# Optimization experiments

Measured on AMD Instinct MI355X. Metric: run time of the kernel, lower is better.

## Reference

```python
import jax, jax.numpy as jnp
import numpy as np

B, T, D, K = 32, 2048, 1024, 31


def setup_inputs() -> dict:
    key = jax.random.key(0)
    ks = jax.random.split(key, 8)
    query = jax.random.normal(ks[0], (B, D), dtype=jnp.float32)
    memory = jax.random.normal(ks[1], (B, T, D), dtype=jnp.float32)
    prev_attn = jax.nn.softmax(jax.random.normal(ks[2], (B, T)), axis=-1).astype(jnp.float32)
    cum_attn = jax.random.uniform(ks[3], (B, T), dtype=jnp.float32)
    mask = jax.random.bernoulli(ks[4], 0.2, (B, T))
    mask = mask.at[:, 0].set(False)  # keep at least one valid position per row
    scale = 0.02
    Wq = jax.random.normal(ks[5], (D, D), dtype=jnp.float32) * scale    # torch Linear weight [out,in]
    Wm = jax.random.normal(ks[6], (D, D), dtype=jnp.float32) * scale
    k2 = jax.random.split(ks[7], 2)
    Wloc = jax.random.normal(k2[0], (D, 2, K), dtype=jnp.float32) * scale  # Conv1d weight [out_ch,in_ch,k]
    v = jax.random.normal(k2[1], (D,), dtype=jnp.float32) * scale          # Linear(d_model,1) weight squeezed
    return {"query": query, "memory": memory, "prev_attn": prev_attn,
            "cum_attn": cum_attn, "mask": mask,
            "Wq": Wq, "Wm": Wm, "Wloc": Wloc, "v": v}


def reference(query, memory, prev_attn, cum_attn, mask, Wq, Wm, Wloc, v):
    pad = Wloc.shape[-1] // 2
    # location features: [B,2,T] conv -> [B,D,T] -> [B,T,D]
    loc_in = jnp.stack([prev_attn, cum_attn], axis=1)
    loc = jax.lax.conv_general_dilated(
        loc_in, Wloc, window_strides=(1,), padding=[(pad, pad)],
        dimension_numbers=("NCW", "OIW", "NCW"))
    loc = jnp.transpose(loc, (0, 2, 1))                 # [B,T,D]
    q = (query @ Wq.T)[:, None, :]                      # [B,1,D]
    m = jnp.einsum("btd,ed->bte", memory, Wm)           # [B,T,D]
    e = jnp.einsum("btd,d->bt", jnp.tanh(q + m + loc), v)  # [B,T]
    e = jnp.where(mask, -jnp.inf, e)
    a = jax.nn.softmax(e, axis=1)                       # [B,T]
    ctx = jnp.einsum("bt,btd->bd", a, memory)           # [B,D]
    return ctx, a
```

## Files before the change

kernel.cpp:

```cpp
#include <hip/hip_runtime.h>
#include <math.h>

#define BATCH 32
#define T 2048
#define D 1024
#define KW 31
#define CPAD 15
#define KEXT 62
#define KTOT 1088
#define BM 256
#define BN 256
#define KSTEP 64
#define NK (KTOT / KSTEP)

typedef __bf16 bf16_8 __attribute__((ext_vector_type(8)));
typedef __bf16 bf16_4 __attribute__((ext_vector_type(4)));
typedef float  f32x4  __attribute__((ext_vector_type(4)));

__device__ __forceinline__ float tanh_fast(float x) {
    return 1.f - 2.f * __builtin_amdgcn_rcpf(__expf(2.f * x) + 1.f);
}

__device__ __forceinline__ void glds16(const void* gsrc, void* ldst) {
    __builtin_amdgcn_global_load_lds(
        (const __attribute__((address_space(1))) unsigned int*)gsrc,
        (__attribute__((address_space(3))) unsigned int*)ldst, 16, 0, 0);
}

#define VM4 asm volatile("s_waitcnt vmcnt(4)" ::: "memory")
#define VM0 asm volatile("s_waitcnt vmcnt(0)" ::: "memory")
#define BAR __builtin_amdgcn_s_barrier()
#define PRIO1 __builtin_amdgcn_s_setprio(1)
#define PRIO0 __builtin_amdgcn_s_setprio(0)

__global__ __launch_bounds__(256) void k_prep_b(const float* __restrict__ Wm,
                                                const float* __restrict__ Wloc,
                                                __bf16* __restrict__ Bext) {
    const int idx = blockIdx.x * 256 + threadIdx.x;
    const int d = idx / (KTOT / 4);
    const int kk = (idx % (KTOT / 4)) * 4;
    bf16_4 o;
    #pragma unroll
    for (int u = 0; u < 4; ++u) {
        const int k = kk + u;
        float val = 0.f;
        if (k < D) val = Wm[(size_t)d * D + k];
        else {
            const int j = k - D;
            if (j < KEXT) {
                const int c = (j >= KW) ? 1 : 0;
                const int kp = j - c * KW;
                val = Wloc[((size_t)d * 2 + c) * KW + kp];
            }
        }
        o[u] = (__bf16)val;
    }
    *(bf16_4*)(Bext + (size_t)d * KTOT + kk) = o;
}

__global__ __launch_bounds__(256) void k_prep_amem(const float* __restrict__ memory,
                                                   __bf16* __restrict__ Amem) {
    const int nvec = BATCH * T * (D / 16);
    for (int idx = blockIdx.x * 256 + threadIdx.x; idx < nvec; idx += gridDim.x * 256) {
        const int row = idx >> 6;
        const int c = (idx & 63) * 16;
        const float* src = memory + (size_t)row * D + c;
        const f32x4 a0 = *(const f32x4*)(src);
        const f32x4 a1 = *(const f32x4*)(src + 4);
        const f32x4 a2 = *(const f32x4*)(src + 8);
        const f32x4 a3 = *(const f32x4*)(src + 12);
        bf16_8 o0, o1;
        #pragma unroll
        for (int u = 0; u < 4; ++u) {
            o0[u] = (__bf16)a0[u]; o0[u + 4] = (__bf16)a1[u];
            o1[u] = (__bf16)a2[u]; o1[u + 4] = (__bf16)a3[u];
        }
        __bf16* dst = Amem + (size_t)row * KTOT + c;
        *(bf16_8*)(dst) = o0;
        *(bf16_8*)(dst + 8) = o1;
    }
}

__global__ __launch_bounds__(256) void k_prep_aloc(const float* __restrict__ prev,
                                                   const float* __restrict__ cum,
                                                   __bf16* __restrict__ Amem) {
    const int idx = blockIdx.x * 256 + threadIdx.x;
    const int row = idx >> 4;
    const int j0 = (idx & 15) * 4;
    const int b = row >> 11;
    const int t = row & (T - 1);
    bf16_4 o;
    #pragma unroll
    for (int u = 0; u < 4; ++u) {
        const int j = j0 + u;
        float val = 0.f;
        if (j < KEXT) {
            const int c = (j >= KW) ? 1 : 0;
            const int kp = j - c * KW;
            const int ts = t + kp - CPAD;
            if (ts >= 0 && ts < T)
                val = (c ? cum : prev)[(size_t)b * T + ts];
        }
        o[u] = (__bf16)val;
    }
    *(bf16_4*)(Amem + (size_t)row * KTOT + D + j0) = o;
}

__global__ __launch_bounds__(256) void k_q(const float* __restrict__ query,
                                           const float* __restrict__ Wq,
                                           float* __restrict__ qout) {
    int b = blockIdx.y;
    int w = threadIdx.x >> 6;
    int lane = threadIdx.x & 63;
    int d = blockIdx.x * 4 + w;
    const float* qrow = query + (size_t)b * D;
    const float* wrow = Wq + (size_t)d * D;
    float s = 0.f;
    #pragma unroll
    for (int i = 0; i < D / 64; ++i) s += qrow[lane + i * 64] * wrow[lane + i * 64];
    #pragma unroll
    for (int off = 32; off > 0; off >>= 1) s += __shfl_down(s, off, 64);
    if (lane == 0) qout[(size_t)b * D + d] = s;
}

__global__ __launch_bounds__(512, 2) void k_gemm_e(
    const __bf16* __restrict__ Amem, const __bf16* __restrict__ Bext,
    const float* __restrict__ qv, const float* __restrict__ vvec,
    float* __restrict__ e_part) {
    __shared__ bf16_8 As[2][2048];
    __shared__ bf16_8 Bs[2][2048];

    const int t0 = blockIdx.x * BM;
    const int d0 = blockIdx.y * BN;
    const int b  = blockIdx.z;
    const int tid  = threadIdx.x;
    const int lane = tid & 63;
    const int w    = tid >> 6;
    const int wm   = w >> 2;
    const int wn   = w & 3;
    const int ml   = lane & 15;
    const int qk   = lane >> 4;

    f32x4 acc[8][4] = {};

    const __bf16* gA[2][2];
    const __bf16* gB[2][2];
    int sA[2][2], sB[2][2];
    #pragma unroll
    for (int h = 0; h < 2; ++h) {
        #pragma unroll
        for (int j = 0; j < 2; ++j) {
            const int idx = j * 8 + w;
            const int p = idx >> 1, kfa = idx & 1;
            const int mf = h * 4 + (p & 3) + (idx & 8);
            const int nf = h * 2 + (p & 1) + (p >> 1) * 4;
            gA[h][j] = Amem + ((size_t)b * T + t0 + mf * 16 + ml) * KTOT + kfa * 32 + qk * 8;
            sA[h][j] = (mf * 2 + kfa) * 64;
            gB[h][j] = Bext + (size_t)(d0 + nf * 16 + ml) * KTOT + kfa * 32 + qk * 8;
            sB[h][j] = (nf * 2 + kfa) * 64;
        }
    }

    bf16_8 areg[4][2];
    bf16_8 breg0[2][2], breg1[2][2];

    auto STG_A = [&](int h, int kcol, bf16_8* dst) {
        glds16(gA[h][0] + kcol, dst + sA[h][0]);
        glds16(gA[h][1] + kcol, dst + sA[h][1]);
    };
    auto STG_B = [&](int h, int kcol, bf16_8* dst) {
        glds16(gB[h][0] + kcol, dst + sB[h][0]);
        glds16(gB[h][1] + kcol, dst + sB[h][1]);
    };
    auto LDA = [&](const bf16_8* buf, int ih) {
        #pragma unroll
        for (int i = 0; i < 4; ++i)
            #pragma unroll
            for (int kf = 0; kf < 2; ++kf)
                areg[i][kf] = buf[((wm * 8 + ih * 4 + i) * 2 + kf) * 64 + lane];
    };
    auto LDB = [&](bf16_8 (&dst)[2][2], const bf16_8* buf, int jh) {
        #pragma unroll
        for (int j = 0; j < 2; ++j)
            #pragma unroll
            for (int kf = 0; kf < 2; ++kf)
                dst[j][kf] = buf[((wn * 4 + jh * 2 + j) * 2 + kf) * 64 + lane];
    };
    auto QMM = [&](bf16_8 (&bb)[2][2], int ih, int jh) {
        #pragma unroll
        for (int i = 0; i < 4; ++i)
            #pragma unroll
            for (int kf = 0; kf < 2; ++kf)
                #pragma unroll
                for (int j = 0; j < 2; ++j)
                    acc[ih * 4 + i][jh * 2 + j] = __builtin_amdgcn_mfma_f32_16x16x32_bf16(
                        areg[i][kf], bb[j][kf], acc[ih * 4 + i][jh * 2 + j], 0, 0, 0);
    };

    STG_A(0, 0, As[0]);
    STG_B(0, 0, Bs[0]);
    STG_B(1, 0, Bs[0]);
    STG_A(1, 0, As[0]);
    VM4;
    BAR;

    #pragma unroll 1
    for (int k = 0; k < NK; ++k) {
        const bf16_8* Ac = As[k & 1];
        const bf16_8* Bc = Bs[k & 1];
        bf16_8* An = As[(k + 1) & 1];
        bf16_8* Bn = Bs[(k + 1) & 1];
        const int c1 = ((k + 1 < NK) ? (k + 1) : 0) * KSTEP;
        LDA(Ac, 0);
        LDB(breg0, Bc, 0);
        STG_A(0, c1, An);
        BAR;
        PRIO1; QMM(breg0, 0, 0); PRIO0;
        VM4;
        BAR;
        LDB(breg1, Bc, 1);
        STG_B(0, c1, Bn);
        BAR;
        PRIO1; QMM(breg1, 0, 1); PRIO0;
        VM4;
        BAR;
        LDA(Ac, 1);
        STG_B(1, c1, Bn);
        BAR;
        PRIO1; QMM(breg0, 1, 0); PRIO0;
        BAR;
        STG_A(1, c1, An);
        BAR;
        PRIO1; QMM(breg1, 1, 1); PRIO0;
        VM4;
        BAR;
    }
    VM0;

    float qreg[4], vreg[4];
    #pragma unroll
    for (int jb = 0; jb < 4; ++jb) {
        const int d = d0 + wn * 64 + jb * 16 + ml;
        qreg[jb] = qv[(size_t)b * D + d];
        vreg[jb] = vvec[d];
    }
    const int dch = blockIdx.y * 4 + wn;
    #pragma unroll
    for (int ia = 0; ia < 8; ++ia) {
        #pragma unroll
        for (int r = 0; r < 4; ++r) {
            float s = 0.f;
            #pragma unroll
            for (int jb = 0; jb < 4; ++jb)
                s += tanh_fast(acc[ia][jb][r] + qreg[jb]) * vreg[jb];
            #pragma unroll
            for (int off = 8; off > 0; off >>= 1)
                s += __shfl_down(s, off, 16);
            if (ml == 0) {
                const int t = t0 + wm * 128 + ia * 16 + qk * 4 + r;
                e_part[((size_t)b * T + t) * 16 + dch] = s;
            }
        }
    }
}

__global__ __launch_bounds__(256) void k_softmax(const float* __restrict__ e_part,
                                                 const int* __restrict__ mask,
                                                 float* __restrict__ aout) {
    const int b = blockIdx.x;
    const int tid = threadIdx.x;
    __shared__ float red[256];
    float ev[8];
    float lmax = -INFINITY;
    #pragma unroll
    for (int i = 0; i < 8; ++i) {
        const int t = tid + i * 256;
        const float* p = e_part + ((size_t)b * T + t) * 16;
        float s = 0.f;
        #pragma unroll
        for (int c = 0; c < 16; ++c) s += p[c];
        if (mask[(size_t)b * T + t] != 0) s = -INFINITY;
        ev[i] = s;
        lmax = fmaxf(lmax, s);
    }
    red[tid] = lmax; __syncthreads();
    for (int off = 128; off > 0; off >>= 1) {
        if (tid < off) red[tid] = fmaxf(red[tid], red[tid + off]);
        __syncthreads();
    }
    const float mx = red[0]; __syncthreads();
    float lsum = 0.f;
    #pragma unroll
    for (int i = 0; i < 8; ++i) {
        const float x = expf(ev[i] - mx);
        ev[i] = x;
        lsum += x;
    }
    red[tid] = lsum; __syncthreads();
    for (int off = 128; off > 0; off >>= 1) {
        if (tid < off) red[tid] += red[tid + off];
        __syncthreads();
    }
    const float inv = 1.f / red[0];
    #pragma unroll
    for (int i = 0; i < 8; ++i)
        aout[(size_t)b * T + tid + i * 256] = ev[i] * inv;
}

__global__ __launch_bounds__(256) void k_ctx_part(const float* __restrict__ memory,
                                                  const float* __restrict__ a,
                                                  float* __restrict__ ctx_part) {
    const int b = blockIdx.x;
    const int tc = blockIdx.y;
    const int d4 = threadIdx.x * 4;
    f32x4 acc = {0.f, 0.f, 0.f, 0.f};
    const float* mb = memory + ((size_t)b * T + (size_t)tc * 64) * D;
    const float* ab = a + (size_t)b * T + (size_t)tc * 64;
    #pragma unroll 4
    for (int t = 0; t < 64; ++t) {
        const float wgt = ab[t];
        const f32x4 m4 = *(const f32x4*)(mb + (size_t)t * D + d4);
        acc += wgt * m4;
    }
    *(f32x4*)(ctx_part + ((size_t)(b * 32 + tc)) * D + d4) = acc;
}

__global__ __launch_bounds__(256) void k_ctx_red(const float* __restrict__ ctx_part,
                                                 float* __restrict__ ctx) {
    const int idx = blockIdx.x * 256 + threadIdx.x;
    const int b = idx >> 10, d = idx & 1023;
    float s = 0.f;
    #pragma unroll
    for (int tc = 0; tc < 32; ++tc) s += ctx_part[((size_t)(b * 32 + tc)) * D + d];
    ctx[idx] = s;
}

extern "C" void kernel_launch(void* const* d_in, const int* in_sizes, int n_in,
                              void* d_out, int out_size, void* d_ws, size_t ws_size,
                              hipStream_t stream) {
    const float* query  = (const float*)d_in[0];
    const float* memory = (const float*)d_in[1];
    const float* prev   = (const float*)d_in[2];
    const float* cum    = (const float*)d_in[3];
    const int*   mask   = (const int*)d_in[4];
    const float* Wq     = (const float*)d_in[5];
    const float* Wm     = (const float*)d_in[6];
    const float* Wloc   = (const float*)d_in[7];
    const float* v      = (const float*)d_in[8];

    float* out = (float*)d_out;
    float* ctx = out;
    float* a   = out + BATCH * D;

    char* ws = (char*)d_ws;
    float*  qv       = (float*)(ws + 0);
    float*  e_part   = (float*)(ws + 131072);
    float*  ctx_part = (float*)(ws + 4325376);
    __bf16* Bext     = (__bf16*)(ws + 8519680);
    __bf16* Amem     = (__bf16*)(ws + 10747904);

    k_prep_b<<<KTOT * D / (256 * 4), 256, 0, stream>>>(Wm, Wloc, Bext);
    k_prep_amem<<<4096, 256, 0, stream>>>(memory, Amem);
    k_prep_aloc<<<BATCH * T * 16 / 256, 256, 0, stream>>>(prev, cum, Amem);
    k_q<<<dim3(D / 4, BATCH), 256, 0, stream>>>(query, Wq, qv);
    k_gemm_e<<<dim3(T / BM, D / BN, BATCH), 512, 0, stream>>>(Amem, Bext, qv, v, e_part);
    k_softmax<<<BATCH, 256, 0, stream>>>(e_part, mask, a);
    k_ctx_part<<<dim3(BATCH, 32), 256, 0, stream>>>(memory, a, ctx_part);
    k_ctx_red<<<(BATCH * D) / 256, 256, 0, stream>>>(ctx_part, ctx);
}
```

Measured before the change: 686.1 us.

## Merge prep kernels, reduce e partials in LDS, read bf16 memory for ctx

Combines the four preprocessing kernels into one launch that dispatches on block index, removing three launches and their tail gaps. In the GEMM epilogue the four per-warp column partials are summed through shared memory, so only 4 partials per row are written instead of 16, and the softmax reads them as one vector. The context kernel now reads the bf16 copy of memory instead of fp32, halving its traffic. The cost is lower context precision and an extra barrier in the GEMM epilogue.

```diff
diff --git a/kernel.cpp b/kernel.cpp
--- a/kernel.cpp
+++ b/kernel.cpp
@@ -33,94 +33,93 @@
 #define PRIO1 __builtin_amdgcn_s_setprio(1)
 #define PRIO0 __builtin_amdgcn_s_setprio(0)
 
-__global__ __launch_bounds__(256) void k_prep_b(const float* __restrict__ Wm,
-                                                const float* __restrict__ Wloc,
-                                                __bf16* __restrict__ Bext) {
-    const int idx = blockIdx.x * 256 + threadIdx.x;
-    const int d = idx / (KTOT / 4);
-    const int kk = (idx % (KTOT / 4)) * 4;
-    bf16_4 o;
-    #pragma unroll
-    for (int u = 0; u < 4; ++u) {
-        const int k = kk + u;
-        float val = 0.f;
-        if (k < D) val = Wm[(size_t)d * D + k];
-        else {
-            const int j = k - D;
-            if (j < KEXT) {
-                const int c = (j >= KW) ? 1 : 0;
-                const int kp = j - c * KW;
-                val = Wloc[((size_t)d * 2 + c) * KW + kp];
+#define PREP_BLOCKS 17472
+__global__ __launch_bounds__(256) void k_prep_all(
+    const float* __restrict__ Wm, const float* __restrict__ Wloc,
+    __bf16* __restrict__ Bext,
+    const float* __restrict__ memory, __bf16* __restrict__ Amem,
+    const float* __restrict__ prev, const float* __restrict__ cum,
+    const float* __restrict__ query, const float* __restrict__ Wq,
+    float* __restrict__ qout) {
+    const int gb = blockIdx.x;
+    if (gb < 4096) {
+        const int nvec = BATCH * T * (D / 16);
+        for (int idx = gb * 256 + threadIdx.x; idx < nvec; idx += 4096 * 256) {
+            const int row = idx >> 6;
+            const int c = (idx & 63) * 16;
+            const float* src = memory + (size_t)row * D + c;
+            const f32x4 a0 = *(const f32x4*)(src);
+            const f32x4 a1 = *(const f32x4*)(src + 4);
+            const f32x4 a2 = *(const f32x4*)(src + 8);
+            const f32x4 a3 = *(const f32x4*)(src + 12);
+            bf16_8 o0, o1;
+            #pragma unroll
+            for (int u = 0; u < 4; ++u) {
+                o0[u] = (__bf16)a0[u]; o0[u + 4] = (__bf16)a1[u];
+                o1[u] = (__bf16)a2[u]; o1[u + 4] = (__bf16)a3[u];
             }
-        }
-        o[u] = (__bf16)val;
-    }
-    *(bf16_4*)(Bext + (size_t)d * KTOT + kk) = o;
-}
-
-__global__ __launch_bounds__(256) void k_prep_amem(const float* __restrict__ memory,
-                                                   __bf16* __restrict__ Amem) {
-    const int nvec = BATCH * T * (D / 16);
-    for (int idx = blockIdx.x * 256 + threadIdx.x; idx < nvec; idx += gridDim.x * 256) {
-        const int row = idx >> 6;
-        const int c = (idx & 63) * 16;
-        const float* src = memory + (size_t)row * D + c;
-        const f32x4 a0 = *(const f32x4*)(src);
-        const f32x4 a1 = *(const f32x4*)(src + 4);
-        const f32x4 a2 = *(const f32x4*)(src + 8);
-        const f32x4 a3 = *(const f32x4*)(src + 12);
-        bf16_8 o0, o1;
+            __bf16* dst = Amem + (size_t)row * KTOT + c;
+            *(bf16_8*)(dst) = o0;
+            *(bf16_8*)(dst + 8) = o1;
+        }
+    } else if (gb < 12288) {
+        const int j = gb - 4096;
+        const int xb = j & 255;
+        const int b = j >> 8;
+        const int w = threadIdx.x >> 6;
+        const int lane = threadIdx.x & 63;
+        const int d = xb * 4 + w;
+        const float* qrow = query + (size_t)b * D;
+        const float* wrow = Wq + (size_t)d * D;
+        float s = 0.f;
+        #pragma unroll
+        for (int i = 0; i < D / 64; ++i) s += qrow[lane + i * 64] * wrow[lane + i * 64];
+        #pragma unroll
+        for (int off = 32; off > 0; off >>= 1) s += __shfl_down(s, off, 64);
+        if (lane == 0) qout[(size_t)b * D + d] = s;
+    } else if (gb < 16384) {
+        const int idx = (gb - 12288) * 256 + threadIdx.x;
+        const int row = idx >> 4;
+        const int j0 = (idx & 15) * 4;
+        const int b = row >> 11;
+        const int t = row & (T - 1);
+        bf16_4 o;
         #pragma unroll
         for (int u = 0; u < 4; ++u) {
-            o0[u] = (__bf16)a0[u]; o0[u + 4] = (__bf16)a1[u];
-            o1[u] = (__bf16)a2[u]; o1[u + 4] = (__bf16)a3[u];
-        }
-        __bf16* dst = Amem + (size_t)row * KTOT + c;
-        *(bf16_8*)(dst) = o0;
-        *(bf16_8*)(dst + 8) = o1;
-    }
-}
-
-__global__ __launch_bounds__(256) void k_prep_aloc(const float* __restrict__ prev,
-                                                   const float* __restrict__ cum,
-                                                   __bf16* __restrict__ Amem) {
-    const int idx = blockIdx.x * 256 + threadIdx.x;
-    const int row = idx >> 4;
-    const int j0 = (idx & 15) * 4;
-    const int b = row >> 11;
-    const int t = row & (T - 1);
-    bf16_4 o;
-    #pragma unroll
-    for (int u = 0; u < 4; ++u) {
-        const int j = j0 + u;
-        float val = 0.f;
-        if (j < KEXT) {
-            const int c = (j >= KW) ? 1 : 0;
-            const int kp = j - c * KW;
-            const int ts = t + kp - CPAD;
-            if (ts >= 0 && ts < T)
-                val = (c ? cum : prev)[(size_t)b * T + ts];
-        }
-        o[u] = (__bf16)val;
-    }
-    *(bf16_4*)(Amem + (size_t)row * KTOT + D + j0) = o;
-}
-
-__global__ __launch_bounds__(256) void k_q(const float* __restrict__ query,
-                                           const float* __restrict__ Wq,
-                                           float* __restrict__ qout) {
-    int b = blockIdx.y;
-    int w = threadIdx.x >> 6;
-    int lane = threadIdx.x & 63;
-    int d = blockIdx.x * 4 + w;
-    const float* qrow = query + (size_t)b * D;
-    const float* wrow = Wq + (size_t)d * D;
-    float s = 0.f;
-    #pragma unroll
-    for (int i = 0; i < D / 64; ++i) s += qrow[lane + i * 64] * wrow[lane + i * 64];
-    #pragma unroll
-    for (int off = 32; off > 0; off >>= 1) s += __shfl_down(s, off, 64);
-    if (lane == 0) qout[(size_t)b * D + d] = s;
+            const int jj = j0 + u;
+            float val = 0.f;
+            if (jj < KEXT) {
+                const int c = (jj >= KW) ? 1 : 0;
+                const int kp = jj - c * KW;
+                const int ts = t + kp - CPAD;
+                if (ts >= 0 && ts < T)
+                    val = (c ? cum : prev)[(size_t)b * T + ts];
+            }
+            o[u] = (__bf16)val;
+        }
+        *(bf16_4*)(Amem + (size_t)row * KTOT + D + j0) = o;
+    } else {
+        const int idx = (gb - 16384) * 256 + threadIdx.x;
+        const int d = idx / (KTOT / 4);
+        const int kk = (idx % (KTOT / 4)) * 4;
+        bf16_4 o;
+        #pragma unroll
+        for (int u = 0; u < 4; ++u) {
+            const int k = kk + u;
+            float val = 0.f;
+            if (k < D) val = Wm[(size_t)d * D + k];
+            else {
+                const int jj = k - D;
+                if (jj < KEXT) {
+                    const int c = (jj >= KW) ? 1 : 0;
+                    const int kp = jj - c * KW;
+                    val = Wloc[((size_t)d * 2 + c) * KW + kp];
+                }
+            }
+            o[u] = (__bf16)val;
+        }
+        *(bf16_4*)(Bext + (size_t)d * KTOT + kk) = o;
+    }
 }
 
 __global__ __launch_bounds__(512, 2) void k_gemm_e(
@@ -236,6 +235,7 @@
         BAR;
     }
     VM0;
+    BAR;
 
     float qreg[4], vreg[4];
     #pragma unroll
@@ -244,7 +244,7 @@
         qreg[jb] = qv[(size_t)b * D + d];
         vreg[jb] = vvec[d];
     }
-    const int dch = blockIdx.y * 4 + wn;
+    float (*est)[256] = (float (*)[256])(&As[0][0]);
     #pragma unroll
     for (int ia = 0; ia < 8; ++ia) {
         #pragma unroll
@@ -256,11 +256,14 @@
             #pragma unroll
             for (int off = 8; off > 0; off >>= 1)
                 s += __shfl_down(s, off, 16);
-            if (ml == 0) {
-                const int t = t0 + wm * 128 + ia * 16 + qk * 4 + r;
-                e_part[((size_t)b * T + t) * 16 + dch] = s;
-            }
-        }
+            if (ml == 0)
+                est[wn][wm * 128 + ia * 16 + qk * 4 + r] = s;
+        }
+    }
+    __syncthreads();
+    if (tid < 256) {
+        const float e = est[0][tid] + est[1][tid] + est[2][tid] + est[3][tid];
+        e_part[((size_t)b * T + t0 + tid) * 4 + blockIdx.y] = e;
     }
 }
 
@@ -275,10 +278,8 @@
     #pragma unroll
     for (int i = 0; i < 8; ++i) {
         const int t = tid + i * 256;
-        const float* p = e_part + ((size_t)b * T + t) * 16;
-        float s = 0.f;
-        #pragma unroll
-        for (int c = 0; c < 16; ++c) s += p[c];
+        const f32x4 p4 = *(const f32x4*)(e_part + ((size_t)b * T + t) * 4);
+        float s = p4[0] + p4[1] + p4[2] + p4[3];
         if (mask[(size_t)b * T + t] != 0) s = -INFINITY;
         ev[i] = s;
         lmax = fmaxf(lmax, s);
@@ -307,20 +308,21 @@
         aout[(size_t)b * T + tid + i * 256] = ev[i] * inv;
 }
 
-__global__ __launch_bounds__(256) void k_ctx_part(const float* __restrict__ memory,
+__global__ __launch_bounds__(256) void k_ctx_part(const __bf16* __restrict__ Amem,
                                                   const float* __restrict__ a,
                                                   float* __restrict__ ctx_part) {
     const int b = blockIdx.x;
     const int tc = blockIdx.y;
     const int d4 = threadIdx.x * 4;
     f32x4 acc = {0.f, 0.f, 0.f, 0.f};
-    const float* mb = memory + ((size_t)b * T + (size_t)tc * 64) * D;
+    const __bf16* mb = Amem + ((size_t)b * T + (size_t)tc * 64) * KTOT + d4;
     const float* ab = a + (size_t)b * T + (size_t)tc * 64;
     #pragma unroll 4
     for (int t = 0; t < 64; ++t) {
         const float wgt = ab[t];
-        const f32x4 m4 = *(const f32x4*)(mb + (size_t)t * D + d4);
-        acc += wgt * m4;
+        const bf16_4 m4 = *(const bf16_4*)(mb + (size_t)t * KTOT);
+        #pragma unroll
+        for (int u = 0; u < 4; ++u) acc[u] += wgt * (float)m4[u];
     }
     *(f32x4*)(ctx_part + ((size_t)(b * 32 + tc)) * D + d4) = acc;
 }
@@ -359,12 +361,10 @@
     __bf16* Bext     = (__bf16*)(ws + 8519680);
     __bf16* Amem     = (__bf16*)(ws + 10747904);
 
-    k_prep_b<<<KTOT * D / (256 * 4), 256, 0, stream>>>(Wm, Wloc, Bext);
-    k_prep_amem<<<4096, 256, 0, stream>>>(memory, Amem);
-    k_prep_aloc<<<BATCH * T * 16 / 256, 256, 0, stream>>>(prev, cum, Amem);
-    k_q<<<dim3(D / 4, BATCH), 256, 0, stream>>>(query, Wq, qv);
+    k_prep_all<<<PREP_BLOCKS, 256, 0, stream>>>(Wm, Wloc, Bext, memory, Amem,
+                                                prev, cum, query, Wq, qv);
     k_gemm_e<<<dim3(T / BM, D / BN, BATCH), 512, 0, stream>>>(Amem, Bext, qv, v, e_part);
     k_softmax<<<BATCH, 256, 0, stream>>>(e_part, mask, a);
-    k_ctx_part<<<dim3(BATCH, 32), 256, 0, stream>>>(memory, a, ctx_part);
+    k_ctx_part<<<dim3(BATCH, 32), 256, 0, stream>>>(Amem, a, ctx_part);
     k_ctx_red<<<(BATCH * D) / 256, 256, 0, stream>>>(ctx_part, ctx);
 }
```

Measured after the change: 641.0 us. -6.6%, faster.
